# Performance work log

Measured on AMD Instinct MI355X. Metric: run time of the kernel, lower is better.

Reference implementation:

```python
import jax, jax.numpy as jnp
import numpy as np

N, E = 30000, 480000
D_IN, D_HID = 128, 256
NODE_CLS, EDGE_CLS, POLAR = 5, 2, 6
EPS = 1e-5

def layer_norm(x, g, b):
    mu = jnp.mean(x, axis=-1, keepdims=True)
    var = jnp.mean((x - mu) ** 2, axis=-1, keepdims=True)
    return g * (x - mu) / jnp.sqrt(var + EPS) + b

def sage_pool(h, src, dst, Wp, bp, Ws, bs, Wn, n_nodes):
    # DGL SAGEConv aggregator_type='pool': m = relu(fc_pool(h_src)); max over in-edges
    m = jax.nn.relu(h @ Wp + bp)              # [N, d_in]
    agg = jax.ops.segment_max(m[src], dst, num_segments=n_nodes)  # [N, d_in], -inf if no in-edges
    deg = jax.ops.segment_sum(jnp.ones((src.shape[0],), jnp.float32), dst, num_segments=n_nodes)
    h_neigh = jnp.where(deg[:, None] > 0, agg, 0.0)
    out = h @ Ws + bs + h_neigh @ Wn          # fc_self + fc_neigh
    return jax.nn.relu(out)                   # activation=F.relu

def setup_inputs() -> dict:
    key = jax.random.key(0)
    ks = jax.random.split(key, 24)
    p = lambda k, shape, fan: jax.random.normal(k, shape, jnp.float32) / np.sqrt(fan)
    return {
        "h": jax.random.normal(ks[0], (N, D_IN), jnp.float32),
        "efeat": jax.random.normal(ks[1], (E, POLAR), jnp.float32),
        "src": jax.random.randint(ks[2], (E,), 0, N, jnp.int32),
        "dst": jax.random.randint(ks[3], (E,), 0, N, jnp.int32),
        # encoder SAGEConv(128->256)
        "enc_Wpool": p(ks[4], (D_IN, D_IN), D_IN), "enc_bpool": jnp.zeros((D_IN,), jnp.float32),
        "enc_Wself": p(ks[5], (D_IN, D_HID), D_IN), "enc_bself": jnp.zeros((D_HID,), jnp.float32),
        "enc_Wneigh": p(ks[6], (D_IN, D_HID), D_IN),
        # node_pred: Linear(256,5) + LayerNorm(5)
        "np_W": p(ks[7], (D_HID, NODE_CLS), D_HID), "np_b": jnp.zeros((NODE_CLS,), jnp.float32),
        "np_g": jnp.ones((NODE_CLS,), jnp.float32), "np_beta": jnp.zeros((NODE_CLS,), jnp.float32),
        # edge predictor: Linear(528,256) + LN(256) + Linear(256,2)
        "ep_W1": p(ks[8], (2 * D_HID + 2 * NODE_CLS + POLAR, D_HID), 2 * D_HID + 16),
        "ep_b1": jnp.zeros((D_HID,), jnp.float32),
        "ep_g": jnp.ones((D_HID,), jnp.float32), "ep_beta": jnp.zeros((D_HID,), jnp.float32),
        "ep_W2": p(ks[9], (D_HID, EDGE_CLS), D_HID), "ep_b2": jnp.zeros((EDGE_CLS,), jnp.float32),
        # decoder SAGEConv(256->128)
        "dec_Wpool": p(ks[10], (D_HID, D_HID), D_HID), "dec_bpool": jnp.zeros((D_HID,), jnp.float32),
        "dec_Wself": p(ks[11], (D_HID, D_IN), D_HID), "dec_bself": jnp.zeros((D_IN,), jnp.float32),
        "dec_Wneigh": p(ks[12], (D_HID, D_IN), D_HID),
    }

def reference(h, efeat, src, dst,
              enc_Wpool, enc_bpool, enc_Wself, enc_bself, enc_Wneigh,
              np_W, np_b, np_g, np_beta,
              ep_W1, ep_b1, ep_g, ep_beta, ep_W2, ep_b2,
              dec_Wpool, dec_bpool, dec_Wself, dec_bself, dec_Wneigh):
    # encoder (drop_rate == 0 path)
    h1 = sage_pool(h, src, dst, enc_Wpool, enc_bpool, enc_Wself, enc_bself, enc_Wneigh, N)
    # node head
    node_pred = layer_norm(h1 @ np_W + np_b, np_g, np_beta)  # [N, 5]
    # edge head: gather-concat-MLP per edge
    cls_sm = jax.nn.softmax(node_pred, axis=1)               # softmax once, gather per edge
    x = jnp.concatenate([h1[src], cls_sm[src], efeat, h1[dst], cls_sm[dst]], axis=1)  # [E, 528]
    x = jax.nn.relu(layer_norm(x @ ep_W1 + ep_b1, ep_g, ep_beta))
    edges_pred = x @ ep_W2 + ep_b2                           # dropout is identity in eval
    # decoder (uses original graph, input h1)
    h2 = sage_pool(h1, src, dst, dec_Wpool, dec_bpool, dec_Wself, dec_bself, dec_Wneigh, N)
    return (node_pred, edges_pred, h2)
```

## Files before the change

### kernel.cpp

```cpp
#include <hip/hip_runtime.h>

typedef unsigned short u16;
typedef unsigned int u32;
typedef __bf16 bf16_t;
typedef bf16_t bf16x8 __attribute__((ext_vector_type(8)));
typedef float f32x4 __attribute__((ext_vector_type(4)));
typedef float f32x2 __attribute__((ext_vector_type(2)));

#define N_NODES 30000
#define N_EDGES 480000

static __device__ __forceinline__ float b2f(u16 u) {
  return __uint_as_float(((u32)u) << 16);
}
static __device__ __forceinline__ float b2f_lo(u32 w) {
  return __uint_as_float(w << 16);
}
static __device__ __forceinline__ float b2f_hi(u32 w) {
  return __uint_as_float(w & 0xffff0000u);
}
static __device__ __forceinline__ u16 f2b(float f) {
  u32 x = __float_as_uint(f);
  u32 r = (x + 0x7fffu + ((x >> 16) & 1u)) >> 16;
  return (u16)r;
}

__global__ __launch_bounds__(256) void init_sniff_deg(const u16* __restrict__ h,
                                                      int* __restrict__ flag,
                                                      int* __restrict__ deg) {
  int i = blockIdx.x * 256 + threadIdx.x;
  if (i < N_NODES) deg[i] = 0;
  if (blockIdx.x == 0) {
    int t = threadIdx.x;
    int bad = 0;
#pragma unroll
    for (int j = 0; j < 4; j++) {
      u32 e = ((u32)h[t * 4 + j] >> 7) & 0xFFu;
      if (e >= 0x8Eu) bad = 1;
    }
    int r = __syncthreads_or(bad);
    if (t == 0) *flag = r ? 1 : 0;
  }
}

struct ConvDesc { const void* s; u16* d; int n; int off; };
struct ConvTab { ConvDesc e[20]; int total; };

__global__ __launch_bounds__(256) void conv_all(
    const int* __restrict__ dstE, int* __restrict__ deg,
    const void* __restrict__ hsrc, u16* __restrict__ c_h,
    const void* __restrict__ efsrc, u16* __restrict__ c_ef,
    ConvTab tab, const int* __restrict__ flag) {
  int b = blockIdx.x;
  const int t = threadIdx.x;
  if (b < 1875) {
    int e = b * 256 + t;
    if (e < N_EDGES) atomicAdd(&deg[dstE[e]], 1);
    return;
  }
  b -= 1875;
  const int f = *flag;
  if (b < 3750) {
    int i = b * 256 + t;
    if (f) {
      float4 v = ((const float4*)hsrc)[i];
      uint2 o;
      o.x = (u32)f2b(v.x) | ((u32)f2b(v.y) << 16);
      o.y = (u32)f2b(v.z) | ((u32)f2b(v.w) << 16);
      ((uint2*)c_h)[i] = o;
    } else {
      ((uint2*)c_h)[i] = ((const uint2*)hsrc)[i];
    }
    return;
  }
  b -= 3750;
  if (b < 2813) {
    int i = b * 256 + t;
    if (i < 720000) {
      if (f) {
        float4 v = ((const float4*)efsrc)[i];
        uint2 o;
        o.x = (u32)f2b(v.x) | ((u32)f2b(v.y) << 16);
        o.y = (u32)f2b(v.z) | ((u32)f2b(v.w) << 16);
        ((uint2*)c_ef)[i] = o;
      } else {
        ((uint2*)c_ef)[i] = ((const uint2*)efsrc)[i];
      }
    }
    return;
  }
  b -= 2813;
  int i = b * 256 + t;
  if (i >= tab.total) return;
#pragma unroll 1
  for (int a = 0; a < 20; a++) {
    int j = i - tab.e[a].off;
    if (j >= 0 && j < tab.e[a].n) {
      if (f) tab.e[a].d[j] = f2b(((const float*)tab.e[a].s)[j]);
      else tab.e[a].d[j] = ((const u16*)tab.e[a].s)[j];
      return;
    }
  }
}

__global__ __launch_bounds__(1024) void scan_off(const int* __restrict__ deg,
                                                 int* __restrict__ off,
                                                 int* __restrict__ cursor, int n) {
  __shared__ int wsum[16];
  const int t = threadIdx.x, lane = t & 63, wv = t >> 6;
  const int CH = 30;
  int base = t * CH;
  int v[CH];
  int s = 0;
#pragma unroll
  for (int j = 0; j < CH; j++) {
    int idx = base + j;
    int d = (idx < n) ? deg[idx] : 0;
    v[j] = s;
    s += d;
  }
  int x = s;
#pragma unroll
  for (int d = 1; d < 64; d <<= 1) {
    int y = __shfl_up(x, d, 64);
    if (lane >= d) x += y;
  }
  if (lane == 63) wsum[wv] = x;
  __syncthreads();
  int wadd = 0;
  for (int w = 0; w < wv; w++) wadd += wsum[w];
  int pref = (x - s) + wadd;
  if (t == 0) off[0] = 0;
#pragma unroll
  for (int j = 0; j < CH; j++) {
    int idx = base + j;
    if (idx < n) {
      int excl = pref + v[j];
      int incl = pref + ((j + 1 < CH) ? v[j + 1] : s);
      cursor[idx] = excl;
      off[idx + 1] = incl;
    }
  }
}

__global__ __launch_bounds__(256) void fill_csr(const int* __restrict__ src,
                                                const int* __restrict__ dst,
                                                int* __restrict__ cursor,
                                                int* __restrict__ esrc, int nE) {
  int e = blockIdx.x * 256 + threadIdx.x;
  if (e >= nE) return;
  int p = atomicAdd(&cursor[dst[e]], 1);
  esrc[p] = src[e];
}

#define MRG(r)                                                    \
  do {                                                            \
    a0 = max(a0, (r).x & 0xffffu); a1 = max(a1, (r).x >> 16);     \
    a2 = max(a2, (r).y & 0xffffu); a3 = max(a3, (r).y >> 16);     \
    a4 = max(a4, (r).z & 0xffffu); a5 = max(a5, (r).z >> 16);     \
    a6 = max(a6, (r).w & 0xffffu); a7 = max(a7, (r).w >> 16);     \
  } while (0)

__global__ __launch_bounds__(256) void agg128(const u16* __restrict__ m,
                                              const int* __restrict__ esrc,
                                              const int* __restrict__ off,
                                              u16* __restrict__ out) {
  int wv = threadIdx.x >> 6, lane = threadIdx.x & 63;
  int qd = lane >> 4, l = lane & 15;
  int n = blockIdx.x * 16 + wv * 4 + qd;
  if (n >= N_NODES) return;
  int i = off[n], s1 = off[n + 1];
  u32 a0 = 0, a1 = 0, a2 = 0, a3 = 0, a4 = 0, a5 = 0, a6 = 0, a7 = 0;
  for (; i + 3 < s1; i += 4) {
    int e0 = esrc[i], e1 = esrc[i + 1], e2 = esrc[i + 2], e3 = esrc[i + 3];
    uint4 r0 = *(const uint4*)(m + (size_t)e0 * 128 + l * 8);
    uint4 r1 = *(const uint4*)(m + (size_t)e1 * 128 + l * 8);
    uint4 r2 = *(const uint4*)(m + (size_t)e2 * 128 + l * 8);
    uint4 r3 = *(const uint4*)(m + (size_t)e3 * 128 + l * 8);
    MRG(r0); MRG(r1); MRG(r2); MRG(r3);
  }
  for (; i < s1; i++) {
    uint4 r0 = *(const uint4*)(m + (size_t)esrc[i] * 128 + l * 8);
    MRG(r0);
  }
  uint4 w;
  w.x = a0 | (a1 << 16); w.y = a2 | (a3 << 16);
  w.z = a4 | (a5 << 16); w.w = a6 | (a7 << 16);
  *(uint4*)(out + (size_t)n * 128 + l * 8) = w;
}

__global__ __launch_bounds__(256) void agg256(const u16* __restrict__ m,
                                              const int* __restrict__ esrc,
                                              const int* __restrict__ off,
                                              u16* __restrict__ out) {
  int wv = threadIdx.x >> 6, lane = threadIdx.x & 63;
  int half = lane >> 5, l = lane & 31;
  int n = blockIdx.x * 8 + wv * 2 + half;
  if (n >= N_NODES) return;
  int i = off[n], s1 = off[n + 1];
  u32 a0 = 0, a1 = 0, a2 = 0, a3 = 0, a4 = 0, a5 = 0, a6 = 0, a7 = 0;
  for (; i + 3 < s1; i += 4) {
    int e0 = esrc[i], e1 = esrc[i + 1], e2 = esrc[i + 2], e3 = esrc[i + 3];
    uint4 r0 = *(const uint4*)(m + (size_t)e0 * 256 + l * 8);
    uint4 r1 = *(const uint4*)(m + (size_t)e1 * 256 + l * 8);
    uint4 r2 = *(const uint4*)(m + (size_t)e2 * 256 + l * 8);
    uint4 r3 = *(const uint4*)(m + (size_t)e3 * 256 + l * 8);
    MRG(r0); MRG(r1); MRG(r2); MRG(r3);
  }
  for (; i < s1; i++) {
    uint4 r0 = *(const uint4*)(m + (size_t)esrc[i] * 256 + l * 8);
    MRG(r0);
  }
  uint4 w;
  w.x = a0 | (a1 << 16); w.y = a2 | (a3 << 16);
  w.z = a4 | (a5 << 16); w.w = a6 | (a7 << 16);
  *(uint4*)(out + (size_t)n * 256 + l * 8) = w;
}
#undef MRG

__global__ __launch_bounds__(256) void prep_weights(
    const u16* __restrict__ encWp, const u16* __restrict__ encWs, const u16* __restrict__ encWn,
    const u16* __restrict__ decWp, const u16* __restrict__ decWs, const u16* __restrict__ decWn,
    const u16* __restrict__ epW1, const u16* __restrict__ epb1,
    u16* __restrict__ wt_encpool, u16* __restrict__ wt_enc,
    u16* __restrict__ wt_decpool, u16* __restrict__ wt_dec,
    u16* __restrict__ wt_UV, u16* __restrict__ b512, float* __restrict__ swsum) {
  int b = blockIdx.x;
  const int t = threadIdx.x;
  if (b < 64) {
    int idx = b * 256 + t; int k = idx >> 7, n = idx & 127;
    wt_encpool[n * 128 + k] = encWp[k * 128 + n]; return;
  }
  b -= 64;
  if (b < 128) {
    int idx = b * 256 + t; int k = idx >> 8, n = idx & 255;
    wt_enc[n * 256 + k] = encWs[k * 256 + n]; return;
  }
  b -= 128;
  if (b < 128) {
    int idx = b * 256 + t; int k = idx >> 8, n = idx & 255;
    wt_enc[n * 256 + 128 + k] = encWn[k * 256 + n]; return;
  }
  b -= 128;
  if (b < 256) {
    int idx = b * 256 + t; int k = idx >> 8, n = idx & 255;
    wt_decpool[n * 256 + k] = decWp[k * 256 + n]; return;
  }
  b -= 256;
  if (b < 128) {
    int idx = b * 256 + t; int k = idx >> 7, n = idx & 127;
    wt_dec[n * 512 + k] = decWs[k * 128 + n]; return;
  }
  b -= 128;
  if (b < 128) {
    int idx = b * 256 + t; int k = idx >> 7, n = idx & 127;
    wt_dec[n * 512 + 256 + k] = decWn[k * 128 + n]; return;
  }
  b -= 128;
  if (b < 512) {
    int n = b, n2 = n & 255, base = (n >= 256) ? 267 : 0;
    for (int kp = t; kp < 288; kp += 256) {
      u16 v = (kp < 261) ? epW1[(size_t)(base + kp) * 256 + n2] : (u16)0;
      wt_UV[(size_t)n * 288 + kp] = v;
    }
    return;
  }
  b -= 512;
  if (b < 2) {
    int i = b * 256 + t;
    b512[i] = (i < 256) ? epb1[i] : (u16)0; return;
  }
  int k = t >> 5, l32 = t & 31;
  if (k < 6) {
    uint4 v = *(const uint4*)(epW1 + (size_t)(261 + k) * 256 + l32 * 8);
    float s = b2f_lo(v.x) + b2f_hi(v.x) + b2f_lo(v.y) + b2f_hi(v.y) +
              b2f_lo(v.z) + b2f_hi(v.z) + b2f_lo(v.w) + b2f_hi(v.w);
#pragma unroll
    for (int m = 1; m < 32; m <<= 1) s += __shfl_xor(s, m, 64);
    if (l32 == 0) swsum[k] = s;
  }
}

__global__ __launch_bounds__(256) void gemm_mfma(
    const u16* __restrict__ A0, const u16* __restrict__ A1, int K0, int K1,
    const u16* __restrict__ Bt, const u16* __restrict__ bias, int do_relu,
    u16* __restrict__ C, float* __restrict__ Cf, const int* __restrict__ flag,
    int M, int Nld) {
  __shared__ __align__(16) u16 As[128 * 40];
  __shared__ __align__(16) u16 Bs[128 * 40];
  const int t = threadIdx.x;
  const int lane = t & 63, wv = t >> 6;
  const int wm = wv & 1, wn = wv >> 1;
  const int r = lane & 15, q = lane >> 4;
  const int bm = blockIdx.x, bn = blockIdx.y;
  const int Ktot = K0 + K1;
  const bool usef = (Cf != nullptr) && (*flag != 0);

  f32x4 acc[4][4];
#pragma unroll
  for (int i = 0; i < 4; i++)
#pragma unroll
    for (int j = 0; j < 4; j++) acc[i][j] = (f32x4){0.f, 0.f, 0.f, 0.f};

  for (int kc = 0; kc < Ktot; kc += 32) {
#pragma unroll
    for (int h = 0; h < 2; h++) {
      int idx = t + h * 256;
      int rr = idx >> 2, qq = idx & 3;
      int rowg = bm * 128 + rr;
      uint4 av = make_uint4(0, 0, 0, 0);
      if (rowg < M) {
        const u16* p = (kc < K0) ? (A0 + (size_t)rowg * K0 + kc)
                                 : (A1 + (size_t)rowg * K1 + (kc - K0));
        av = *(const uint4*)(p + qq * 8);
      }
      *(uint4*)&As[rr * 40 + qq * 8] = av;
      int ng = bn * 128 + rr;
      uint4 bv = *(const uint4*)(Bt + (size_t)ng * Ktot + kc + qq * 8);
      *(uint4*)&Bs[rr * 40 + qq * 8] = bv;
    }
    __syncthreads();
    bf16x8 af[4], bfm[4];
#pragma unroll
    for (int mi = 0; mi < 4; mi++)
      af[mi] = *(const bf16x8*)&As[(wm * 64 + mi * 16 + r) * 40 + q * 8];
#pragma unroll
    for (int ni = 0; ni < 4; ni++)
      bfm[ni] = *(const bf16x8*)&Bs[(wn * 64 + ni * 16 + r) * 40 + q * 8];
#pragma unroll
    for (int mi = 0; mi < 4; mi++)
#pragma unroll
      for (int ni = 0; ni < 4; ni++)
        acc[mi][ni] = __builtin_amdgcn_mfma_f32_16x16x32_bf16(af[mi], bfm[ni], acc[mi][ni], 0, 0, 0);
    __syncthreads();
  }

  float bv[4];
#pragma unroll
  for (int ni = 0; ni < 4; ni++)
    bv[ni] = bias ? b2f(bias[bn * 128 + wn * 64 + ni * 16 + r]) : 0.f;
#pragma unroll
  for (int mi = 0; mi < 4; mi++) {
#pragma unroll
    for (int i = 0; i < 4; i++) {
      int rowg = bm * 128 + wm * 64 + mi * 16 + q * 4 + i;
      if (rowg >= M) continue;
#pragma unroll
      for (int ni = 0; ni < 4; ni++) {
        int colg = bn * 128 + wn * 64 + ni * 16 + r;
        float v = acc[mi][ni][i] + bv[ni];
        if (do_relu) v = v > 0.f ? v : 0.f;
        if (usef) Cf[(size_t)rowg * Nld + colg] = v;
        else C[(size_t)rowg * Nld + colg] = f2b(v);
      }
    }
  }
}

__global__ __launch_bounds__(256) void node_head(
    const u16* __restrict__ h1, const u16* __restrict__ W, const u16* __restrict__ b,
    const u16* __restrict__ g, const u16* __restrict__ beta,
    u16* __restrict__ outN, float* __restrict__ outNf, const int* __restrict__ flag,
    u16* __restrict__ smOut) {
  __shared__ float Wl[256 * 5];
  __shared__ float bl[5], gl[5], betal[5];
  int t = threadIdx.x;
#pragma unroll
  for (int c = 0; c < 5; c++) Wl[t * 5 + c] = b2f(W[t * 5 + c]);
  if (t < 5) { bl[t] = b2f(b[t]); gl[t] = b2f(g[t]); betal[t] = b2f(beta[t]); }
  __syncthreads();
  int n = blockIdx.x * 256 + t;
  if (n >= N_NODES) return;
  const bool usef = (*flag != 0);
  float acc[5] = {0.f, 0.f, 0.f, 0.f, 0.f};
  const u16* hp = h1 + (size_t)n * 256;
  for (int k8 = 0; k8 < 32; k8++) {
    uint4 v = *(const uint4*)(hp + k8 * 8);
    u32 wds[4] = {v.x, v.y, v.z, v.w};
#pragma unroll
    for (int h = 0; h < 4; h++) {
      float x0 = b2f_lo(wds[h]), x1 = b2f_hi(wds[h]);
      int k = k8 * 8 + h * 2;
#pragma unroll
      for (int c = 0; c < 5; c++)
        acc[c] += x0 * Wl[k * 5 + c] + x1 * Wl[(k + 1) * 5 + c];
    }
  }
  float x[5], mu = 0.f;
#pragma unroll
  for (int c = 0; c < 5; c++) { x[c] = acc[c] + bl[c]; mu += x[c]; }
  mu *= 0.2f;
  float var = 0.f;
#pragma unroll
  for (int c = 0; c < 5; c++) { float d = x[c] - mu; var += d * d; }
  var *= 0.2f;
  float rstd = rsqrtf(fmaxf(var, 0.f) + 1e-5f);
  float v5[5], mx = -1e30f;
#pragma unroll
  for (int c = 0; c < 5; c++) {
    v5[c] = gl[c] * (x[c] - mu) * rstd + betal[c];
    if (usef) outNf[(size_t)n * 5 + c] = v5[c];
    else outN[(size_t)n * 5 + c] = f2b(v5[c]);
    mx = fmaxf(mx, v5[c]);
  }
  float s = 0.f, ex[5];
#pragma unroll
  for (int c = 0; c < 5; c++) { ex[c] = __expf(v5[c] - mx); s += ex[c]; }
  float inv = 1.f / s;
  u16 row[32];
#pragma unroll
  for (int c = 0; c < 5; c++) row[c] = f2b(ex[c] * inv);
#pragma unroll
  for (int c = 5; c < 32; c++) row[c] = 0;
#pragma unroll
  for (int c = 0; c < 4; c++)
    *(uint4*)(smOut + (size_t)n * 32 + c * 8) = *(const uint4*)&row[c * 8];
}

__global__ __launch_bounds__(256) void rowsum_uv(const u16* __restrict__ UV,
                                                 float2* __restrict__ Srow) {
  int wv = threadIdx.x >> 6, lane = threadIdx.x & 63;
  int n = blockIdx.x * 4 + wv;
  if (n >= N_NODES) return;
  uint4 v = *(const uint4*)(UV + (size_t)n * 512 + lane * 8);
  float s = b2f_lo(v.x) + b2f_hi(v.x) + b2f_lo(v.y) + b2f_hi(v.y) +
            b2f_lo(v.z) + b2f_hi(v.z) + b2f_lo(v.w) + b2f_hi(v.w);
#pragma unroll
  for (int m = 1; m < 32; m <<= 1) s += __shfl_xor(s, m, 64);
  if (lane == 0) Srow[n].x = s;
  if (lane == 32) Srow[n].y = s;
}

__global__ __launch_bounds__(256) void edge_mean(
    const int* __restrict__ src, const int* __restrict__ dst,
    const u16* __restrict__ ef, const float2* __restrict__ Srow,
    const float* __restrict__ swsum, uint4* __restrict__ recs) {
  int p = blockIdx.x * 256 + threadIdx.x;
  if (p >= 240000) {
    if (p < 240016) {
      uint4 z = make_uint4(0, 0, 0, 0);
      recs[(size_t)p * 3 + 0] = z;
      recs[(size_t)p * 3 + 1] = z;
      recs[(size_t)p * 3 + 2] = z;
    }
    return;
  }
  int e = p * 2;
  int s0 = src[e], s1 = src[e + 1];
  int d0 = dst[e], d1 = dst[e + 1];
  const u32* efp = (const u32*)(ef + (size_t)e * 6);
  u32 f0 = efp[0], f1 = efp[1], f2 = efp[2], f3 = efp[3], f4 = efp[4], f5 = efp[5];
  float xa[6] = {b2f_lo(f0), b2f_hi(f0), b2f_lo(f1), b2f_hi(f1), b2f_lo(f2), b2f_hi(f2)};
  float xb[6] = {b2f_lo(f3), b2f_hi(f3), b2f_lo(f4), b2f_hi(f4), b2f_lo(f5), b2f_hi(f5)};
  float sw[6];
#pragma unroll
  for (int k = 0; k < 6; k++) sw[k] = swsum[k];
  float m0 = Srow[s0].x + Srow[d0].y;
  float m1 = Srow[s1].x + Srow[d1].y;
#pragma unroll
  for (int k = 0; k < 6; k++) { m0 += xa[k] * sw[k]; m1 += xb[k] * sw[k]; }
  m0 *= (1.f / 256.f);
  m1 *= (1.f / 256.f);
  uint4 ra, rb, rc;
  ra.x = (u32)s0; ra.y = (u32)d0; ra.z = (u32)s1; ra.w = (u32)d1;
  rb.x = __float_as_uint(m0); rb.y = __float_as_uint(m1); rb.z = f0; rb.w = f1;
  rc.x = f2; rc.y = f3; rc.z = f4; rc.w = f5;
  recs[(size_t)p * 3 + 0] = ra;
  recs[(size_t)p * 3 + 1] = rb;
  recs[(size_t)p * 3 + 2] = rc;
}

__global__ __launch_bounds__(256) void edge_pt(
    const u16* __restrict__ UV, const uint4* __restrict__ recs,
    const u16* __restrict__ w1raw,
    const u16* __restrict__ g, const u16* __restrict__ beta,
    const u16* __restrict__ w2, const u16* __restrict__ b2,
    u16* __restrict__ outE, float* __restrict__ outEf, const int* __restrict__ flag) {
  const int t = threadIdx.x;
  const int lane = t & 63, wv = t >> 6;
  const int c0 = lane * 4;
  const int grp = (lane >> 4) & 3;
  f32x2 wefA[6], wefB[6];
#pragma unroll
  for (int k = 0; k < 6; k++) {
    u32 wa = *(const u32*)(w1raw + (size_t)(261 + k) * 256 + c0);
    u32 wb = *(const u32*)(w1raw + (size_t)(261 + k) * 256 + c0 + 2);
    wefA[k] = (f32x2){b2f_lo(wa), b2f_hi(wa)};
    wefB[k] = (f32x2){b2f_lo(wb), b2f_hi(wb)};
  }
  f32x2 glA = (f32x2){b2f(g[c0]), b2f(g[c0 + 1])};
  f32x2 glB = (f32x2){b2f(g[c0 + 2]), b2f(g[c0 + 3])};
  f32x2 blA = (f32x2){b2f(beta[c0]), b2f(beta[c0 + 1])};
  f32x2 blB = (f32x2){b2f(beta[c0 + 2]), b2f(beta[c0 + 3])};
  float w20[4], w21[4];
#pragma unroll
  for (int j = 0; j < 4; j++) {
    w20[j] = b2f(w2[(c0 + j) * 2]); w21[j] = b2f(w2[(c0 + j) * 2 + 1]);
  }
  const float b20 = b2f(b2[0]), b21 = b2f(b2[1]);
  const float bsel = (grp & 1) ? b21 : b20;
  const bool usef = (*flag != 0);
  const f32x2 zero2 = (f32x2){0.f, 0.f};

  const int pb = __builtin_amdgcn_readfirstlane((blockIdx.x * 4 + wv) * 16);
  const uint4* rp = recs + (size_t)pb * 3;
  uint4 r0a = rp[0], r0b = rp[1], r0c = rp[2];
  uint4 r1a = rp[3], r1b = rp[4], r1c = rp[5];
  uint2 gua = *(const uint2*)(UV + ((size_t)r0a.x << 9) + c0);
  uint2 gva = *(const uint2*)(UV + ((size_t)r0a.y << 9) + 256 + c0);
  uint2 gub = *(const uint2*)(UV + ((size_t)r0a.z << 9) + c0);
  uint2 gvb = *(const uint2*)(UV + ((size_t)r0a.w << 9) + 256 + c0);
#pragma unroll 2
  for (int it = 0; it < 16; ++it) {
    const int e = (pb + it) * 2;
    uint2 hua = *(const uint2*)(UV + ((size_t)r1a.x << 9) + c0);
    uint2 hva = *(const uint2*)(UV + ((size_t)r1a.y << 9) + 256 + c0);
    uint2 hub = *(const uint2*)(UV + ((size_t)r1a.z << 9) + c0);
    uint2 hvb = *(const uint2*)(UV + ((size_t)r1a.w << 9) + 256 + c0);
    uint4 r2a = rp[3 * it + 6], r2b = rp[3 * it + 7], r2c = rp[3 * it + 8];

    const float ma = __uint_as_float(r0b.x), mb = __uint_as_float(r0b.y);
    float xa[6] = {b2f_lo(r0b.z), b2f_hi(r0b.z), b2f_lo(r0b.w), b2f_hi(r0b.w),
                   b2f_lo(r0c.x), b2f_hi(r0c.x)};
    float xb[6] = {b2f_lo(r0c.y), b2f_hi(r0c.y), b2f_lo(r0c.z), b2f_hi(r0c.z),
                   b2f_lo(r0c.w), b2f_hi(r0c.w)};

    f32x2 yaA = (f32x2){b2f_lo(gua.x), b2f_hi(gua.x)} + (f32x2){b2f_lo(gva.x), b2f_hi(gva.x)};
    f32x2 yaB = (f32x2){b2f_lo(gua.y), b2f_hi(gua.y)} + (f32x2){b2f_lo(gva.y), b2f_hi(gva.y)};
    f32x2 ybA = (f32x2){b2f_lo(gub.x), b2f_hi(gub.x)} + (f32x2){b2f_lo(gvb.x), b2f_hi(gvb.x)};
    f32x2 ybB = (f32x2){b2f_lo(gub.y), b2f_hi(gub.y)} + (f32x2){b2f_lo(gvb.y), b2f_hi(gvb.y)};
#pragma unroll
    for (int k = 0; k < 6; k++) {
      yaA += xa[k] * wefA[k];
      yaB += xa[k] * wefB[k];
      ybA += xb[k] * wefA[k];
      ybB += xb[k] * wefB[k];
    }
    float pqa = yaA.x * yaA.x;
    pqa += yaA.y * yaA.y; pqa += yaB.x * yaB.x; pqa += yaB.y * yaB.y;
    float pqb = ybA.x * ybA.x;
    pqb += ybA.y * ybA.y; pqb += ybB.x * ybB.x; pqb += ybB.y * ybB.y;
    pqa += __shfl_xor(pqa, 32, 64);
    pqb += __shfl_xor(pqb, 32, 64);
    float z = (lane < 32) ? pqa : pqb;
#pragma unroll
    for (int m = 16; m >= 1; m >>= 1) z += __shfl_xor(z, m, 64);
    float zz = __shfl_xor(z, 32, 64);
    float pqa_t = (lane < 32) ? z : zz;
    float pqb_t = (lane < 32) ? zz : z;
    float rsa = rsqrtf(fmaxf(pqa_t * (1.f / 256.f) - ma * ma, 0.f) + 1e-5f);
    float rsb = rsqrtf(fmaxf(pqb_t * (1.f / 256.f) - mb * mb, 0.f) + 1e-5f);
    f32x2 nAa = __builtin_elementwise_max((yaA - ma) * rsa * glA + blA, zero2);
    f32x2 nAb = __builtin_elementwise_max((yaB - ma) * rsa * glB + blB, zero2);
    f32x2 nBa = __builtin_elementwise_max((ybA - mb) * rsb * glA + blA, zero2);
    f32x2 nBb = __builtin_elementwise_max((ybB - mb) * rsb * glB + blB, zero2);
    float p0a = nAa.x * w20[0], p1a = nAa.x * w21[0];
    p0a += nAa.y * w20[1]; p1a += nAa.y * w21[1];
    p0a += nAb.x * w20[2]; p1a += nAb.x * w21[2];
    p0a += nAb.y * w20[3]; p1a += nAb.y * w21[3];
    float p0b = nBa.x * w20[0], p1b = nBa.x * w21[0];
    p0b += nBa.y * w20[1]; p1b += nBa.y * w21[1];
    p0b += nBb.x * w20[2]; p1b += nBb.x * w21[2];
    p0b += nBb.y * w20[3]; p1b += nBb.y * w21[3];
    p0a += __shfl_xor(p0a, 32, 64); p1a += __shfl_xor(p1a, 32, 64);
    p0b += __shfl_xor(p0b, 32, 64); p1b += __shfl_xor(p1b, 32, 64);
    p0a += __shfl_xor(p0a, 16, 64); p1a += __shfl_xor(p1a, 16, 64);
    p0b += __shfl_xor(p0b, 16, 64); p1b += __shfl_xor(p1b, 16, 64);
    float w = (grp & 2) ? ((grp & 1) ? p1b : p0b) : ((grp & 1) ? p1a : p0a);
#pragma unroll
    for (int m = 8; m >= 1; m >>= 1) w += __shfl_xor(w, m, 64);
    if ((lane & 15) == 0) {
      float val = w + bsel;
      size_t oi = (size_t)e * 2 + grp;
      if (usef) outEf[oi] = val;
      else outE[oi] = f2b(val);
    }
    r0a = r1a; r0b = r1b; r0c = r1c;
    r1a = r2a; r1b = r2b; r1c = r2c;
    gua = hua; gva = hva; gub = hub; gvb = hvb;
  }
}

extern "C" void kernel_launch(void* const* d_in, const int* in_sizes, int n_in,
                              void* d_out, int out_size, void* d_ws, size_t ws_size,
                              hipStream_t stream) {
  char* wp = (char*)d_ws;
  auto alloc = [&](size_t bytes) -> char* {
    char* p = wp; wp += (bytes + 255) & ~(size_t)255; return p;
  };
  int* flag       = (int*)alloc(256);
  u16* c_h        = (u16*)alloc((size_t)N_NODES * 128 * 2);
  u16* c_ef       = (u16*)alloc((size_t)N_EDGES * 6 * 2);
  static const int pidx[20] = {4,5,6,7,8, 9,10,11,12, 13,14,15,16,17,18, 19,20,21,22,23};
  static const int pn[20]   = {16384,128,32768,256,32768, 1280,5,5,5,
                               135168,256,256,256,512,2, 65536,256,32768,128,32768};
  u16* cp[20];
  for (int a = 0; a < 20; a++) cp[a] = (u16*)alloc((size_t)pn[a] * 2);

  u16* wt_encpool = (u16*)alloc(128 * 128 * 2);
  u16* wt_enc     = (u16*)alloc(256 * 256 * 2);
  u16* wt_decpool = (u16*)alloc(256 * 256 * 2);
  u16* wt_dec     = (u16*)alloc(128 * 512 * 2);
  u16* wt_UV      = (u16*)alloc(512 * 288 * 2);
  u16* b512       = (u16*)alloc(512 * 2);
  float2* Srow    = (float2*)alloc((size_t)N_NODES * 8);
  float* swsum_b  = (float*)alloc(64);
  u16* m_buf      = (u16*)alloc((size_t)N_NODES * 256 * 2);
  u16* aggb       = (u16*)alloc((size_t)N_NODES * 256 * 2);
  u16* UVbuf      = m_buf;
  u16* h1b        = (u16*)alloc((size_t)N_NODES * 256 * 2);
  u16* smb32      = (u16*)alloc((size_t)N_NODES * 32 * 2);
  int* deg        = (int*)alloc((size_t)N_NODES * 4);
  int* off        = (int*)alloc((size_t)(N_NODES + 1) * 4);
  int* cursor     = (int*)alloc((size_t)N_NODES * 4);
  int* esrc       = (int*)alloc((size_t)N_EDGES * 4);
  uint4* recs     = (uint4*)alloc(((size_t)240000 * 3 + 64) * 16);

  const int* src = (const int*)d_in[2];
  const int* dst = (const int*)d_in[3];

  u16* outN = (u16*)d_out;
  u16* outE = outN + (size_t)N_NODES * 5;
  u16* outH = outN + 1110000;
  float* outNf = (float*)d_out;
  float* outEf = outNf + (size_t)N_NODES * 5;
  float* outHf = outNf + 1110000;

  init_sniff_deg<<<118, 256, 0, stream>>>((const u16*)d_in[0], flag, deg);
  ConvTab tab;
  int off_a = 0;
  for (int a = 0; a < 20; a++) {
    tab.e[a].s = d_in[pidx[a]]; tab.e[a].d = cp[a]; tab.e[a].n = pn[a]; tab.e[a].off = off_a;
    off_a += pn[a];
  }
  tab.total = off_a;
  int conv_blocks = 1875 + 3750 + 2813 + (off_a + 255) / 256;
  conv_all<<<conv_blocks, 256, 0, stream>>>(dst, deg, d_in[0], c_h, d_in[1], c_ef, tab, flag);

  const u16 *enc_Wpool = cp[0], *enc_bpool = cp[1], *enc_Wself = cp[2], *enc_bself = cp[3],
            *enc_Wneigh = cp[4], *np_W = cp[5], *np_b = cp[6], *np_g = cp[7], *np_beta = cp[8],
            *ep_W1 = cp[9], *ep_b1 = cp[10], *ep_g = cp[11], *ep_beta = cp[12],
            *ep_W2 = cp[13], *ep_b2 = cp[14], *dec_Wpool = cp[15], *dec_bpool = cp[16],
            *dec_Wself = cp[17], *dec_bself = cp[18], *dec_Wneigh = cp[19];

  scan_off<<<1, 1024, 0, stream>>>(deg, off, cursor, N_NODES);
  fill_csr<<<1875, 256, 0, stream>>>(src, dst, cursor, esrc, N_EDGES);

  prep_weights<<<1347, 256, 0, stream>>>(enc_Wpool, enc_Wself, enc_Wneigh,
                                         dec_Wpool, dec_Wself, dec_Wneigh,
                                         ep_W1, ep_b1,
                                         wt_encpool, wt_enc, wt_decpool, wt_dec,
                                         wt_UV, b512, swsum_b);

  gemm_mfma<<<dim3(235, 1), 256, 0, stream>>>(c_h, nullptr, 128, 0, wt_encpool,
                                              enc_bpool, 1, m_buf, nullptr, flag, N_NODES, 128);
  agg128<<<1875, 256, 0, stream>>>(m_buf, esrc, off, aggb);
  gemm_mfma<<<dim3(235, 2), 256, 0, stream>>>(c_h, aggb, 128, 128, wt_enc,
                                              enc_bself, 1, h1b, nullptr, flag, N_NODES, 256);
  node_head<<<118, 256, 0, stream>>>(h1b, np_W, np_b, np_g, np_beta, outN, outNf, flag, smb32);
  gemm_mfma<<<dim3(235, 4), 256, 0, stream>>>(h1b, smb32, 256, 32, wt_UV,
                                              b512, 0, UVbuf, nullptr, flag, N_NODES, 512);
  rowsum_uv<<<7500, 256, 0, stream>>>(UVbuf, Srow);
  edge_mean<<<938, 256, 0, stream>>>(src, dst, c_ef, Srow, swsum_b, recs);
  edge_pt<<<3750, 256, 0, stream>>>(UVbuf, recs, ep_W1, ep_g, ep_beta, ep_W2, ep_b2,
                                    outE, outEf, flag);
  gemm_mfma<<<dim3(235, 2), 256, 0, stream>>>(h1b, nullptr, 256, 0, wt_decpool,
                                              dec_bpool, 1, m_buf, nullptr, flag, N_NODES, 256);
  agg256<<<3750, 256, 0, stream>>>(m_buf, esrc, off, aggb);
  gemm_mfma<<<dim3(235, 1), 256, 0, stream>>>(h1b, aggb, 256, 256, wt_dec,
                                              dec_bself, 1, outH, outHf, flag, N_NODES, 128);
}
```

Baseline: 467.4 us.

## Merge independent stages into combined launches to overlap decoder work with edge head

Fuses CSR fill with weight prep, node head with the decoder pool GEMM, the UV GEMM with part of the decoder aggregation, and the edge MLP with the rest of the decoder aggregation. Blocks are interleaved inside each combined kernel. The aim is to remove launch gaps and let memory-bound gather work run alongside compute-heavy work. The edge kernel also drops its two-deep prefetch of UV rows for a simpler one-step record prefetch, which may expose more gather latency. UV now gets its own buffer, and dec_m reuses enc_m with a larger row width, so it relies on enc_m and enc_agg being contiguous.

```diff
diff --git a/kernel.cpp b/kernel.cpp
--- a/kernel.cpp
+++ b/kernel.cpp
@@ -9,6 +9,7 @@
 
 #define N_NODES 30000
 #define N_EDGES 480000
+#define AGG_EARLY 768
 
 static __device__ __forceinline__ float b2f(u16 u) {
   return __uint_as_float(((u32)u) << 16);
@@ -143,14 +144,88 @@
   }
 }
 
-__global__ __launch_bounds__(256) void fill_csr(const int* __restrict__ src,
-                                                const int* __restrict__ dst,
-                                                int* __restrict__ cursor,
-                                                int* __restrict__ esrc, int nE) {
-  int e = blockIdx.x * 256 + threadIdx.x;
-  if (e >= nE) return;
-  int p = atomicAdd(&cursor[dst[e]], 1);
-  esrc[p] = src[e];
+static __device__ void prep_body(
+    int b, int t,
+    const u16* __restrict__ encWp, const u16* __restrict__ encWs, const u16* __restrict__ encWn,
+    const u16* __restrict__ decWp, const u16* __restrict__ decWs, const u16* __restrict__ decWn,
+    const u16* __restrict__ epW1, const u16* __restrict__ epb1,
+    u16* __restrict__ wt_encpool, u16* __restrict__ wt_enc,
+    u16* __restrict__ wt_decpool, u16* __restrict__ wt_dec,
+    u16* __restrict__ wt_UV, u16* __restrict__ b512, float* __restrict__ swsum) {
+  if (b < 64) {
+    int idx = b * 256 + t; int k = idx >> 7, n = idx & 127;
+    wt_encpool[n * 128 + k] = encWp[k * 128 + n]; return;
+  }
+  b -= 64;
+  if (b < 128) {
+    int idx = b * 256 + t; int k = idx >> 8, n = idx & 255;
+    wt_enc[n * 256 + k] = encWs[k * 256 + n]; return;
+  }
+  b -= 128;
+  if (b < 128) {
+    int idx = b * 256 + t; int k = idx >> 8, n = idx & 255;
+    wt_enc[n * 256 + 128 + k] = encWn[k * 256 + n]; return;
+  }
+  b -= 128;
+  if (b < 256) {
+    int idx = b * 256 + t; int k = idx >> 8, n = idx & 255;
+    wt_decpool[n * 256 + k] = decWp[k * 256 + n]; return;
+  }
+  b -= 256;
+  if (b < 128) {
+    int idx = b * 256 + t; int k = idx >> 7, n = idx & 127;
+    wt_dec[n * 512 + k] = decWs[k * 128 + n]; return;
+  }
+  b -= 128;
+  if (b < 128) {
+    int idx = b * 256 + t; int k = idx >> 7, n = idx & 127;
+    wt_dec[n * 512 + 256 + k] = decWn[k * 128 + n]; return;
+  }
+  b -= 128;
+  if (b < 512) {
+    int n = b, n2 = n & 255, base = (n >= 256) ? 267 : 0;
+    for (int kp = t; kp < 288; kp += 256) {
+      u16 v = (kp < 261) ? epW1[(size_t)(base + kp) * 256 + n2] : (u16)0;
+      wt_UV[(size_t)n * 288 + kp] = v;
+    }
+    return;
+  }
+  b -= 512;
+  if (b < 2) {
+    int i = b * 256 + t;
+    b512[i] = (i < 256) ? epb1[i] : (u16)0; return;
+  }
+  int k = t >> 5, l32 = t & 31;
+  if (k < 6) {
+    uint4 v = *(const uint4*)(epW1 + (size_t)(261 + k) * 256 + l32 * 8);
+    float s = b2f_lo(v.x) + b2f_hi(v.x) + b2f_lo(v.y) + b2f_hi(v.y) +
+              b2f_lo(v.z) + b2f_hi(v.z) + b2f_lo(v.w) + b2f_hi(v.w);
+#pragma unroll
+    for (int m = 1; m < 32; m <<= 1) s += __shfl_xor(s, m, 64);
+    if (l32 == 0) swsum[k] = s;
+  }
+}
+
+__global__ __launch_bounds__(256) void fill_prep(
+    const int* __restrict__ src, const int* __restrict__ dst,
+    int* __restrict__ cursor, int* __restrict__ esrc,
+    const u16* __restrict__ encWp, const u16* __restrict__ encWs, const u16* __restrict__ encWn,
+    const u16* __restrict__ decWp, const u16* __restrict__ decWs, const u16* __restrict__ decWn,
+    const u16* __restrict__ epW1, const u16* __restrict__ epb1,
+    u16* __restrict__ wt_encpool, u16* __restrict__ wt_enc,
+    u16* __restrict__ wt_decpool, u16* __restrict__ wt_dec,
+    u16* __restrict__ wt_UV, u16* __restrict__ b512, float* __restrict__ swsum) {
+  int b = blockIdx.x;
+  if (b < 1875) {
+    int e = b * 256 + threadIdx.x;
+    if (e < N_EDGES) {
+      int p = atomicAdd(&cursor[dst[e]], 1);
+      esrc[p] = src[e];
+    }
+    return;
+  }
+  prep_body(b - 1875, threadIdx.x, encWp, encWs, encWn, decWp, decWs, decWn,
+            epW1, epb1, wt_encpool, wt_enc, wt_decpool, wt_dec, wt_UV, b512, swsum);
 }
 
 #define MRG(r)                                                    \
@@ -189,13 +264,13 @@
   *(uint4*)(out + (size_t)n * 128 + l * 8) = w;
 }
 
-__global__ __launch_bounds__(256) void agg256(const u16* __restrict__ m,
-                                              const int* __restrict__ esrc,
-                                              const int* __restrict__ off,
-                                              u16* __restrict__ out) {
+static __device__ void agg256_body(const u16* __restrict__ m,
+                                   const int* __restrict__ esrc,
+                                   const int* __restrict__ off,
+                                   u16* __restrict__ out, int blk) {
   int wv = threadIdx.x >> 6, lane = threadIdx.x & 63;
   int half = lane >> 5, l = lane & 31;
-  int n = blockIdx.x * 8 + wv * 2 + half;
+  int n = blk * 8 + wv * 2 + half;
   if (n >= N_NODES) return;
   int i = off[n], s1 = off[n + 1];
   u32 a0 = 0, a1 = 0, a2 = 0, a3 = 0, a4 = 0, a5 = 0, a6 = 0, a7 = 0;
@@ -218,81 +293,16 @@
 }
 #undef MRG
 
-__global__ __launch_bounds__(256) void prep_weights(
-    const u16* __restrict__ encWp, const u16* __restrict__ encWs, const u16* __restrict__ encWn,
-    const u16* __restrict__ decWp, const u16* __restrict__ decWs, const u16* __restrict__ decWn,
-    const u16* __restrict__ epW1, const u16* __restrict__ epb1,
-    u16* __restrict__ wt_encpool, u16* __restrict__ wt_enc,
-    u16* __restrict__ wt_decpool, u16* __restrict__ wt_dec,
-    u16* __restrict__ wt_UV, u16* __restrict__ b512, float* __restrict__ swsum) {
-  int b = blockIdx.x;
-  const int t = threadIdx.x;
-  if (b < 64) {
-    int idx = b * 256 + t; int k = idx >> 7, n = idx & 127;
-    wt_encpool[n * 128 + k] = encWp[k * 128 + n]; return;
-  }
-  b -= 64;
-  if (b < 128) {
-    int idx = b * 256 + t; int k = idx >> 8, n = idx & 255;
-    wt_enc[n * 256 + k] = encWs[k * 256 + n]; return;
-  }
-  b -= 128;
-  if (b < 128) {
-    int idx = b * 256 + t; int k = idx >> 8, n = idx & 255;
-    wt_enc[n * 256 + 128 + k] = encWn[k * 256 + n]; return;
-  }
-  b -= 128;
-  if (b < 256) {
-    int idx = b * 256 + t; int k = idx >> 8, n = idx & 255;
-    wt_decpool[n * 256 + k] = decWp[k * 256 + n]; return;
-  }
-  b -= 256;
-  if (b < 128) {
-    int idx = b * 256 + t; int k = idx >> 7, n = idx & 127;
-    wt_dec[n * 512 + k] = decWs[k * 128 + n]; return;
-  }
-  b -= 128;
-  if (b < 128) {
-    int idx = b * 256 + t; int k = idx >> 7, n = idx & 127;
-    wt_dec[n * 512 + 256 + k] = decWn[k * 128 + n]; return;
-  }
-  b -= 128;
-  if (b < 512) {
-    int n = b, n2 = n & 255, base = (n >= 256) ? 267 : 0;
-    for (int kp = t; kp < 288; kp += 256) {
-      u16 v = (kp < 261) ? epW1[(size_t)(base + kp) * 256 + n2] : (u16)0;
-      wt_UV[(size_t)n * 288 + kp] = v;
-    }
-    return;
-  }
-  b -= 512;
-  if (b < 2) {
-    int i = b * 256 + t;
-    b512[i] = (i < 256) ? epb1[i] : (u16)0; return;
-  }
-  int k = t >> 5, l32 = t & 31;
-  if (k < 6) {
-    uint4 v = *(const uint4*)(epW1 + (size_t)(261 + k) * 256 + l32 * 8);
-    float s = b2f_lo(v.x) + b2f_hi(v.x) + b2f_lo(v.y) + b2f_hi(v.y) +
-              b2f_lo(v.z) + b2f_hi(v.z) + b2f_lo(v.w) + b2f_hi(v.w);
-#pragma unroll
-    for (int m = 1; m < 32; m <<= 1) s += __shfl_xor(s, m, 64);
-    if (l32 == 0) swsum[k] = s;
-  }
-}
-
-__global__ __launch_bounds__(256) void gemm_mfma(
+static __device__ void gemm_body(
+    int bm, int bn,
     const u16* __restrict__ A0, const u16* __restrict__ A1, int K0, int K1,
     const u16* __restrict__ Bt, const u16* __restrict__ bias, int do_relu,
     u16* __restrict__ C, float* __restrict__ Cf, const int* __restrict__ flag,
-    int M, int Nld) {
-  __shared__ __align__(16) u16 As[128 * 40];
-  __shared__ __align__(16) u16 Bs[128 * 40];
+    int M, int Nld, u16* As, u16* Bs) {
   const int t = threadIdx.x;
   const int lane = t & 63, wv = t >> 6;
   const int wm = wv & 1, wn = wv >> 1;
   const int r = lane & 15, q = lane >> 4;
-  const int bm = blockIdx.x, bn = blockIdx.y;
   const int Ktot = K0 + K1;
   const bool usef = (Cf != nullptr) && (*flag != 0);
 
@@ -357,19 +367,32 @@
   }
 }
 
-__global__ __launch_bounds__(256) void node_head(
+__global__ __launch_bounds__(256) void gemm_mfma(
+    const u16* __restrict__ A0, const u16* __restrict__ A1, int K0, int K1,
+    const u16* __restrict__ Bt, const u16* __restrict__ bias, int do_relu,
+    u16* __restrict__ C, float* __restrict__ Cf, const int* __restrict__ flag,
+    int M, int Nld) {
+  __shared__ __align__(16) u16 As[128 * 40];
+  __shared__ __align__(16) u16 Bs[128 * 40];
+  gemm_body(blockIdx.x, blockIdx.y, A0, A1, K0, K1, Bt, bias, do_relu,
+            C, Cf, flag, M, Nld, As, Bs);
+}
+
+static __device__ void node_head_body(
     const u16* __restrict__ h1, const u16* __restrict__ W, const u16* __restrict__ b,
     const u16* __restrict__ g, const u16* __restrict__ beta,
     u16* __restrict__ outN, float* __restrict__ outNf, const int* __restrict__ flag,
-    u16* __restrict__ smOut) {
-  __shared__ float Wl[256 * 5];
-  __shared__ float bl[5], gl[5], betal[5];
+    u16* __restrict__ smOut, int blk, float* fs) {
+  float* Wl = fs;
+  float* bl = fs + 1280;
+  float* gl = fs + 1285;
+  float* betal = fs + 1290;
   int t = threadIdx.x;
 #pragma unroll
   for (int c = 0; c < 5; c++) Wl[t * 5 + c] = b2f(W[t * 5 + c]);
   if (t < 5) { bl[t] = b2f(b[t]); gl[t] = b2f(g[t]); betal[t] = b2f(beta[t]); }
   __syncthreads();
-  int n = blockIdx.x * 256 + t;
+  int n = blk * 256 + t;
   if (n >= N_NODES) return;
   const bool usef = (*flag != 0);
   float acc[5] = {0.f, 0.f, 0.f, 0.f, 0.f};
@@ -415,6 +438,44 @@
 #pragma unroll
   for (int c = 0; c < 4; c++)
     *(uint4*)(smOut + (size_t)n * 32 + c * 8) = *(const uint4*)&row[c * 8];
+}
+
+__global__ __launch_bounds__(256) void merge_nh_gemm(
+    const u16* __restrict__ h1,
+    const u16* __restrict__ npW, const u16* __restrict__ npb,
+    const u16* __restrict__ npg, const u16* __restrict__ npbeta,
+    u16* __restrict__ outN, float* __restrict__ outNf, const int* __restrict__ flag,
+    u16* __restrict__ smOut,
+    const u16* __restrict__ wt_decpool, const u16* __restrict__ dec_bpool,
+    u16* __restrict__ dec_m) {
+  __shared__ __align__(16) u16 As[128 * 40];
+  __shared__ __align__(16) u16 Bs[128 * 40];
+  __shared__ __align__(16) float NHs[1296];
+  int b = blockIdx.x;
+  if (b < 118) {
+    node_head_body(h1, npW, npb, npg, npbeta, outN, outNf, flag, smOut, b, NHs);
+    return;
+  }
+  b -= 118;
+  gemm_body(b % 235, b / 235, h1, nullptr, 256, 0, wt_decpool, dec_bpool, 1,
+            dec_m, nullptr, flag, N_NODES, 256, As, Bs);
+}
+
+__global__ __launch_bounds__(256) void merge_uv_agg(
+    const u16* __restrict__ h1, const u16* __restrict__ smb32,
+    const u16* __restrict__ wt_UV, const u16* __restrict__ b512,
+    u16* __restrict__ UV, const int* __restrict__ flag,
+    const u16* __restrict__ dec_m, const int* __restrict__ esrc,
+    const int* __restrict__ off, u16* __restrict__ dec_agg) {
+  __shared__ __align__(16) u16 As[128 * 40];
+  __shared__ __align__(16) u16 Bs[128 * 40];
+  int b = blockIdx.x;
+  if (b < 940) {
+    gemm_body(b % 235, b / 235, h1, smb32, 256, 32, wt_UV, b512, 0,
+              UV, nullptr, flag, N_NODES, 512, As, Bs);
+    return;
+  }
+  agg256_body(dec_m, esrc, off, dec_agg, b - 940);
 }
 
 __global__ __launch_bounds__(256) void rowsum_uv(const u16* __restrict__ UV,
@@ -470,12 +531,13 @@
   recs[(size_t)p * 3 + 2] = rc;
 }
 
-__global__ __launch_bounds__(256) void edge_pt(
+static __device__ void edge_pt_body(
     const u16* __restrict__ UV, const uint4* __restrict__ recs,
     const u16* __restrict__ w1raw,
     const u16* __restrict__ g, const u16* __restrict__ beta,
     const u16* __restrict__ w2, const u16* __restrict__ b2,
-    u16* __restrict__ outE, float* __restrict__ outEf, const int* __restrict__ flag) {
+    u16* __restrict__ outE, float* __restrict__ outEf, const int* __restrict__ flag,
+    int blk) {
   const int t = threadIdx.x;
   const int lane = t & 63, wv = t >> 6;
   const int c0 = lane * 4;
@@ -502,33 +564,29 @@
   const bool usef = (*flag != 0);
   const f32x2 zero2 = (f32x2){0.f, 0.f};
 
-  const int pb = __builtin_amdgcn_readfirstlane((blockIdx.x * 4 + wv) * 16);
+  const int pb = __builtin_amdgcn_readfirstlane((blk * 4 + wv) * 16);
   const uint4* rp = recs + (size_t)pb * 3;
-  uint4 r0a = rp[0], r0b = rp[1], r0c = rp[2];
-  uint4 r1a = rp[3], r1b = rp[4], r1c = rp[5];
-  uint2 gua = *(const uint2*)(UV + ((size_t)r0a.x << 9) + c0);
-  uint2 gva = *(const uint2*)(UV + ((size_t)r0a.y << 9) + 256 + c0);
-  uint2 gub = *(const uint2*)(UV + ((size_t)r0a.z << 9) + c0);
-  uint2 gvb = *(const uint2*)(UV + ((size_t)r0a.w << 9) + 256 + c0);
-#pragma unroll 2
+  uint4 ra = rp[0], rb = rp[1], rc = rp[2];
+#pragma unroll 1
   for (int it = 0; it < 16; ++it) {
     const int e = (pb + it) * 2;
-    uint2 hua = *(const uint2*)(UV + ((size_t)r1a.x << 9) + c0);
-    uint2 hva = *(const uint2*)(UV + ((size_t)r1a.y << 9) + 256 + c0);
-    uint2 hub = *(const uint2*)(UV + ((size_t)r1a.z << 9) + c0);
-    uint2 hvb = *(const uint2*)(UV + ((size_t)r1a.w << 9) + 256 + c0);
-    uint4 r2a = rp[3 * it + 6], r2b = rp[3 * it + 7], r2c = rp[3 * it + 8];
-
-    const float ma = __uint_as_float(r0b.x), mb = __uint_as_float(r0b.y);
-    float xa[6] = {b2f_lo(r0b.z), b2f_hi(r0b.z), b2f_lo(r0b.w), b2f_hi(r0b.w),
-                   b2f_lo(r0c.x), b2f_hi(r0c.x)};
-    float xb[6] = {b2f_lo(r0c.y), b2f_hi(r0c.y), b2f_lo(r0c.z), b2f_hi(r0c.z),
-                   b2f_lo(r0c.w), b2f_hi(r0c.w)};
-
-    f32x2 yaA = (f32x2){b2f_lo(gua.x), b2f_hi(gua.x)} + (f32x2){b2f_lo(gva.x), b2f_hi(gva.x)};
-    f32x2 yaB = (f32x2){b2f_lo(gua.y), b2f_hi(gua.y)} + (f32x2){b2f_lo(gva.y), b2f_hi(gva.y)};
-    f32x2 ybA = (f32x2){b2f_lo(gub.x), b2f_hi(gub.x)} + (f32x2){b2f_lo(gvb.x), b2f_hi(gvb.x)};
-    f32x2 ybB = (f32x2){b2f_lo(gub.y), b2f_hi(gub.y)} + (f32x2){b2f_lo(gvb.y), b2f_hi(gvb.y)};
+    uint4 ca = ra, cb = rb, cc = rc;
+    ra = rp[3 * it + 3]; rb = rp[3 * it + 4]; rc = rp[3 * it + 5];
+    const int s0 = (int)ca.x, d0 = (int)ca.y, s1 = (int)ca.z, d1 = (int)ca.w;
+    const float ma = __uint_as_float(cb.x), mb = __uint_as_float(cb.y);
+    float xa[6] = {b2f_lo(cb.z), b2f_hi(cb.z), b2f_lo(cb.w), b2f_hi(cb.w),
+                   b2f_lo(cc.x), b2f_hi(cc.x)};
+    float xb[6] = {b2f_lo(cc.y), b2f_hi(cc.y), b2f_lo(cc.z), b2f_hi(cc.z),
+                   b2f_lo(cc.w), b2f_hi(cc.w)};
+    uint2 ua = *(const uint2*)(UV + ((size_t)(u32)s0 << 9) + c0);
+    uint2 va = *(const uint2*)(UV + ((size_t)(u32)d0 << 9) + 256 + c0);
+    uint2 ub = *(const uint2*)(UV + ((size_t)(u32)s1 << 9) + c0);
+    uint2 vb = *(const uint2*)(UV + ((size_t)(u32)d1 << 9) + 256 + c0);
+
+    f32x2 yaA = (f32x2){b2f_lo(ua.x), b2f_hi(ua.x)} + (f32x2){b2f_lo(va.x), b2f_hi(va.x)};
+    f32x2 yaB = (f32x2){b2f_lo(ua.y), b2f_hi(ua.y)} + (f32x2){b2f_lo(va.y), b2f_hi(va.y)};
+    f32x2 ybA = (f32x2){b2f_lo(ub.x), b2f_hi(ub.x)} + (f32x2){b2f_lo(vb.x), b2f_hi(vb.x)};
+    f32x2 ybB = (f32x2){b2f_lo(ub.y), b2f_hi(ub.y)} + (f32x2){b2f_lo(vb.y), b2f_hi(vb.y)};
 #pragma unroll
     for (int k = 0; k < 6; k++) {
       yaA += xa[k] * wefA[k];
@@ -575,10 +633,27 @@
       if (usef) outEf[oi] = val;
       else outE[oi] = f2b(val);
     }
-    r0a = r1a; r0b = r1b; r0c = r1c;
-    r1a = r2a; r1b = r2b; r1c = r2c;
-    gua = hua; gva = hva; gub = hub; gvb = hvb;
-  }
+  }
+}
+
+__global__ __launch_bounds__(256) void merge_edge_agg(
+    const u16* __restrict__ UV, const uint4* __restrict__ recs,
+    const u16* __restrict__ w1raw,
+    const u16* __restrict__ g, const u16* __restrict__ beta,
+    const u16* __restrict__ w2, const u16* __restrict__ b2,
+    u16* __restrict__ outE, float* __restrict__ outEf, const int* __restrict__ flag,
+    const u16* __restrict__ dec_m, const int* __restrict__ esrc,
+    const int* __restrict__ off, u16* __restrict__ dec_agg) {
+  const int NA = 3750 - AGG_EARLY;
+  int b = blockIdx.x;
+  int task, sub;
+  if (b < 2 * NA) { task = b & 1; sub = b >> 1; }
+  else { task = 0; sub = NA + (b - 2 * NA); }
+  if (task == 1) {
+    agg256_body(dec_m, esrc, off, dec_agg, AGG_EARLY + sub);
+    return;
+  }
+  edge_pt_body(UV, recs, w1raw, g, beta, w2, b2, outE, outEf, flag, sub);
 }
 
 extern "C" void kernel_launch(void* const* d_in, const int* in_sizes, int n_in,
@@ -605,9 +680,11 @@
   u16* b512       = (u16*)alloc(512 * 2);
   float2* Srow    = (float2*)alloc((size_t)N_NODES * 8);
   float* swsum_b  = (float*)alloc(64);
-  u16* m_buf      = (u16*)alloc((size_t)N_NODES * 256 * 2);
-  u16* aggb       = (u16*)alloc((size_t)N_NODES * 256 * 2);
-  u16* UVbuf      = m_buf;
+  u16* enc_m      = (u16*)alloc((size_t)N_NODES * 128 * 2);
+  u16* enc_agg    = (u16*)alloc((size_t)N_NODES * 128 * 2);
+  u16* dec_m      = enc_m;
+  u16* dec_agg    = (u16*)alloc((size_t)N_NODES * 256 * 2);
+  u16* UVbuf      = (u16*)alloc((size_t)N_NODES * 512 * 2);
   u16* h1b        = (u16*)alloc((size_t)N_NODES * 256 * 2);
   u16* smb32      = (u16*)alloc((size_t)N_NODES * 32 * 2);
   int* deg        = (int*)alloc((size_t)N_NODES * 4);
@@ -644,29 +721,28 @@
             *dec_Wself = cp[17], *dec_bself = cp[18], *dec_Wneigh = cp[19];
 
   scan_off<<<1, 1024, 0, stream>>>(deg, off, cursor, N_NODES);
-  fill_csr<<<1875, 256, 0, stream>>>(src, dst, cursor, esrc, N_EDGES);
-
-  prep_weights<<<1347, 256, 0, stream>>>(enc_Wpool, enc_Wself, enc_Wneigh,
-                                         dec_Wpool, dec_Wself, dec_Wneigh,
-                                         ep_W1, ep_b1,
-                                         wt_encpool, wt_enc, wt_decpool, wt_dec,
-                                         wt_UV, b512, swsum_b);
+  fill_prep<<<1875 + 1347, 256, 0, stream>>>(src, dst, cursor, esrc,
+                                             enc_Wpool, enc_Wself, enc_Wneigh,
+                                             dec_Wpool, dec_Wself, dec_Wneigh,
+                                             ep_W1, ep_b1,
+                                             wt_encpool, wt_enc, wt_decpool, wt_dec,
+                                             wt_UV, b512, swsum_b);
 
   gemm_mfma<<<dim3(235, 1), 256, 0, stream>>>(c_h, nullptr, 128, 0, wt_encpool,
-                                              enc_bpool, 1, m_buf, nullptr, flag, N_NODES, 128);
-  agg128<<<1875, 256, 0, stream>>>(m_buf, esrc, off, aggb);
-  gemm_mfma<<<dim3(235, 2), 256, 0, stream>>>(c_h, aggb, 128, 128, wt_enc,
+                                              enc_bpool, 1, enc_m, nullptr, flag, N_NODES, 128);
+  agg128<<<1875, 256, 0, stream>>>(enc_m, esrc, off, enc_agg);
+  gemm_mfma<<<dim3(235, 2), 256, 0, stream>>>(c_h, enc_agg, 128, 128, wt_enc,
                                               enc_bself, 1, h1b, nullptr, flag, N_NODES, 256);
-  node_head<<<118, 256, 0, stream>>>(h1b, np_W, np_b, np_g, np_beta, outN, outNf, flag, smb32);
-  gemm_mfma<<<dim3(235, 4), 256, 0, stream>>>(h1b, smb32, 256, 32, wt_UV,
-                                              b512, 0, UVbuf, nullptr, flag, N_NODES, 512);
+  merge_nh_gemm<<<118 + 470, 256, 0, stream>>>(h1b, np_W, np_b, np_g, np_beta,
+                                               outN, outNf, flag, smb32,
+                                               wt_decpool, dec_bpool, dec_m);
+  merge_uv_agg<<<940 + AGG_EARLY, 256, 0, stream>>>(h1b, smb32, wt_UV, b512, UVbuf, flag,
+                                                    dec_m, esrc, off, dec_agg);
   rowsum_uv<<<7500, 256, 0, stream>>>(UVbuf, Srow);
   edge_mean<<<938, 256, 0, stream>>>(src, dst, c_ef, Srow, swsum_b, recs);
-  edge_pt<<<3750, 256, 0, stream>>>(UVbuf, recs, ep_W1, ep_g, ep_beta, ep_W2, ep_b2,
-                                    outE, outEf, flag);
-  gemm_mfma<<<dim3(235, 2), 256, 0, stream>>>(h1b, nullptr, 256, 0, wt_decpool,
-                                              dec_bpool, 1, m_buf, nullptr, flag, N_NODES, 256);
-  agg256<<<3750, 256, 0, stream>>>(m_buf, esrc, off, aggb);
-  gemm_mfma<<<dim3(235, 1), 256, 0, stream>>>(h1b, aggb, 256, 256, wt_dec,
+  merge_edge_agg<<<2 * (3750 - AGG_EARLY) + AGG_EARLY, 256, 0, stream>>>(
+      UVbuf, recs, ep_W1, ep_g, ep_beta, ep_W2, ep_b2, outE, outEf, flag,
+      dec_m, esrc, off, dec_agg);
+  gemm_mfma<<<dim3(235, 1), 256, 0, stream>>>(h1b, dec_agg, 256, 256, wt_dec,
                                               dec_bself, 1, outH, outHf, flag, N_NODES, 128);
 }
```

After: 535.7 us. 14.6% more time.
